# Performance work log

Hardware: AMD Instinct MI355X
Metric: run time of the kernel (lower is better)

Reference implementation:

```python
import jax, jax.numpy as jnp
import numpy as np

DIM = 1024
HEADS = 16
HEAD_DIM = DIM // HEADS
HIDDEN = 4 * DIM
SCALE = HEAD_DIM ** -0.5
MASK_VAL = -65504.0
EPS = 1e-5


def layernorm(x, scale, bias):
    mu = jnp.mean(x, axis=-1, keepdims=True)
    var = jnp.mean(jnp.square(x - mu), axis=-1, keepdims=True)
    return (x - mu) * jax.lax.rsqrt(var + EPS) * scale + bias


def setup_inputs() -> dict:
    key = jax.random.key(0)
    ks = jax.random.split(key, 10)
    B, N = 2, 2048
    s = 0.02
    return {
        "x": jax.random.normal(ks[0], (B, N, DIM), jnp.float32),
        "attention_mask": jax.random.randint(ks[1], (B, N), 0, 2) > 0,
        "attention_bias": jax.random.normal(ks[2], (N, N), jnp.float32),
        "qkv_w": jax.random.normal(ks[3], (3 * DIM, DIM), jnp.float32) * s,
        "q_bias": jnp.zeros((DIM,), jnp.float32),
        "v_bias": jnp.zeros((DIM,), jnp.float32),
        "proj_w": jax.random.normal(ks[4], (DIM, DIM), jnp.float32) * s,
        "proj_b": jnp.zeros((DIM,), jnp.float32),
        "ln1_s": jnp.ones((DIM,), jnp.float32),
        "ln1_b": jnp.zeros((DIM,), jnp.float32),
        "ln2_s": jnp.ones((DIM,), jnp.float32),
        "ln2_b": jnp.zeros((DIM,), jnp.float32),
        "fc1_w": jax.random.normal(ks[5], (HIDDEN, DIM), jnp.float32) * s,
        "fc1_b": jnp.zeros((HIDDEN,), jnp.float32),
        "fc2_w": jax.random.normal(ks[6], (DIM, HIDDEN), jnp.float32) * s,
        "fc2_b": jnp.zeros((DIM,), jnp.float32),
    }


def reference(x, attention_mask, attention_bias, qkv_w, q_bias, v_bias,
              proj_w, proj_b, ln1_s, ln1_b, ln2_s, ln2_b,
              fc1_w, fc1_b, fc2_w, fc2_b):
    B, N, C = x.shape
    h = layernorm(x, ln1_s, ln1_b)
    qkv_bias = jnp.concatenate([q_bias, jnp.zeros_like(v_bias), v_bias])
    qkv = h @ qkv_w.T + qkv_bias  # [B,N,3C]
    qkv = qkv.reshape(B, N, 3, HEADS, HEAD_DIM).transpose(2, 0, 3, 1, 4)
    q, k, v = qkv[0], qkv[1], qkv[2]  # [B,H,N,D]
    attn = jnp.einsum('bhnd,bhmd->bhnm', q * SCALE, k)
    mask = attention_mask[:, None, None, :]  # [B,1,1,N]
    attn = jnp.where(mask, MASK_VAL, attn)
    attn = attn + attention_bias[None, None]  # [1,1,N,N] bias
    attn = jax.nn.softmax(attn, axis=-1)
    out = jnp.einsum('bhnm,bhmd->bnhd', attn, v).reshape(B, N, C)
    x_attn = out @ proj_w.T + proj_b
    x = x + x_attn
    h2 = layernorm(x, ln2_s, ln2_b)
    h2 = jax.nn.gelu(h2 @ fc1_w.T + fc1_b, approximate=False)
    x = x + (h2 @ fc2_w.T + fc2_b)
    return (x, attn)
```

## Files before the change

kernel.cpp:

```cpp
#include <hip/hip_runtime.h>
#include <hip/hip_bf16.h>
#include <math.h>

#define NTOK 2048
#define DIM  1024
#define SCALE 0.125f
#define MASK_VAL -65504.0f

typedef __attribute__((ext_vector_type(8))) short bf16x8;
typedef __attribute__((ext_vector_type(4))) float floatx4;

#define MFMA16(a,b,c) __builtin_amdgcn_mfma_f32_16x16x32_bf16((a),(b),(c),0,0,0)
#define GLL16(g,l) __builtin_amdgcn_global_load_lds( \
    (const __attribute__((address_space(1))) void*)(g), \
    (__attribute__((address_space(3))) void*)(l), 16, 0, 0)

__device__ __forceinline__ short f2bf(float f) {
  union { __hip_bfloat16 h; short s; } u;
  u.h = __float2bfloat16(f);
  return u.s;
}
__device__ __forceinline__ float bf2f(short s) {
  union { short s; __hip_bfloat16 h; } u;
  u.s = s;
  return __bfloat162float(u.h);
}

__global__ __launch_bounds__(256) void cvt_bf16(const float* __restrict__ in,
                                                short* __restrict__ out) {
  size_t i = ((size_t)blockIdx.x * 256 + threadIdx.x) * 4;
  float4 v = *(const float4*)(in + i);
  short4 o;
  o.x = f2bf(v.x); o.y = f2bf(v.y); o.z = f2bf(v.z); o.w = f2bf(v.w);
  *(short4*)(out + i) = o;
}

__global__ __launch_bounds__(256) void ln_k(const float* __restrict__ x,
                                            const float* __restrict__ sc,
                                            const float* __restrict__ bi,
                                            short* __restrict__ out) {
  int row = blockIdx.x, t = threadIdx.x;
  float4 v = ((const float4*)(x + (size_t)row * DIM))[t];
  float s  = v.x + v.y + v.z + v.w;
  float s2 = v.x*v.x + v.y*v.y + v.z*v.z + v.w*v.w;
#pragma unroll
  for (int off = 32; off; off >>= 1) {
    s  += __shfl_xor(s, off);
    s2 += __shfl_xor(s2, off);
  }
  __shared__ float ps[4], ps2[4];
  if ((t & 63) == 0) { ps[t >> 6] = s; ps2[t >> 6] = s2; }
  __syncthreads();
  s  = ps[0] + ps[1] + ps[2] + ps[3];
  s2 = ps2[0] + ps2[1] + ps2[2] + ps2[3];
  float mu  = s * (1.0f / DIM);
  float inv = rsqrtf(s2 * (1.0f / DIM) - mu * mu + 1e-5f);
  float4 g = ((const float4*)sc)[t], b = ((const float4*)bi)[t];
  short4 o;
  o.x = f2bf((v.x - mu) * inv * g.x + b.x);
  o.y = f2bf((v.y - mu) * inv * g.y + b.y);
  o.z = f2bf((v.z - mu) * inv * g.z + b.z);
  o.w = f2bf((v.w - mu) * inv * g.w + b.w);
  ((short4*)(out + (size_t)row * DIM))[t] = o;
}

enum { E_QKV = 0, E_RESID = 1, E_FC1 = 2 };

template <int EPI, int K, int BN>
__global__ __launch_bounds__(256) void gemm_bt(
    const short* __restrict__ A, const short* __restrict__ B,
    const float* __restrict__ bias0, const float* __restrict__ bias1,
    const float* __restrict__ resid, float* __restrict__ outf,
    short* __restrict__ o0, short* __restrict__ o1, short* __restrict__ o2) {
  __shared__ short As[128 * 32];
  __shared__ short Bs[BN * 32];
  constexpr int MI = (BN == 128) ? 4 : 2;
  const int t = threadIdx.x;
  const int bm = blockIdx.x, bn = blockIdx.y;
  const int l = t & 63, w = t >> 6;
  const int lr = l & 15, lh = l >> 4;
  const int rowbase = (BN == 128) ? (w >> 1) * 64 : w * 32;
  const int colbase = (BN == 128) ? (w & 1) * 64 : 0;

  const short* ga = A + (size_t)(bm * 128 + (t >> 2)) * K + (t & 3) * 8;
  const short* gb = B + (size_t)(bn * BN + (t >> 2)) * K + (t & 3) * 8;
  short* la = As + t * 8;
  short* lb = Bs + t * 8;

  floatx4 acc[MI][4] = {};
  for (int kb = 0; kb < K / 32; ++kb) {
    GLL16(ga, la);
    GLL16(ga + (size_t)64 * K, la + 2048);
    GLL16(gb, lb);
    if constexpr (BN == 128) GLL16(gb + (size_t)64 * K, lb + 2048);
    ga += 32; gb += 32;
    __syncthreads();
    bf16x8 af[MI], bfr[4];
#pragma unroll
    for (int m = 0; m < MI; m++)
      af[m] = *(const bf16x8*)(As + (rowbase + m * 16 + lr) * 32 + lh * 8);
#pragma unroll
    for (int n = 0; n < 4; n++)
      bfr[n] = *(const bf16x8*)(Bs + (colbase + n * 16 + lr) * 32 + lh * 8);
#pragma unroll
    for (int m = 0; m < MI; m++)
#pragma unroll
      for (int n = 0; n < 4; n++)
        acc[m][n] = MFMA16(af[m], bfr[n], acc[m][n]);
    __syncthreads();
  }

#pragma unroll
  for (int m = 0; m < MI; m++) {
#pragma unroll
    for (int n = 0; n < 4; n++) {
#pragma unroll
      for (int j = 0; j < 4; j++) {
        int gr = bm * 128 + rowbase + m * 16 + lh * 4 + j;
        int gc = bn * BN + colbase + n * 16 + lr;
        float val = acc[m][n][j];
        if constexpr (EPI == E_QKV) {
          int which = gc >> 10, d = gc & 1023;
          int bb = gr >> 11, n_ = gr & 2047;
          size_t idx = (((size_t)bb * 16 + (d >> 6)) * NTOK + n_) * 64 + (d & 63);
          if (which == 0)      o0[idx] = f2bf((val + bias0[d]) * SCALE);
          else if (which == 1) o1[idx] = f2bf(val);
          else                 o2[idx] = f2bf(val + bias1[d]);
        } else if constexpr (EPI == E_RESID) {
          size_t idx = (size_t)gr * 1024 + gc;
          outf[idx] = val + bias0[gc] + resid[idx];
        } else {
          float u = val + bias0[gc];
          float gelu = 0.5f * u * (1.0f + erff(u * 0.70710678f));
          o0[(size_t)gr * 4096 + gc] = f2bf(gelu);
        }
      }
    }
  }
}

__global__ __launch_bounds__(256) void transpose_v(const short* __restrict__ v,
                                                   short* __restrict__ vt) {
  __shared__ short tile[64][72];
  int bh = blockIdx.x, nb = blockIdx.y, t = threadIdx.x;
  int r = t >> 2, c0 = (t & 3) * 16;
  const short* src = v + ((size_t)bh * NTOK + nb * 64 + r) * 64 + c0;
  *(bf16x8*)&tile[r][c0]     = *(const bf16x8*)src;
  *(bf16x8*)&tile[r][c0 + 8] = *(const bf16x8*)(src + 8);
  __syncthreads();
  int d = t >> 2, n0 = (t & 3) * 16;
  bf16x8 a, b;
#pragma unroll
  for (int i = 0; i < 8; i++) { a[i] = tile[n0 + i][d]; b[i] = tile[n0 + 8 + i][d]; }
  short* dst = vt + ((size_t)bh * 64 + d) * NTOK + nb * 64 + n0;
  *(bf16x8*)dst       = a;
  *(bf16x8*)(dst + 8) = b;
}

__global__ __launch_bounds__(512) void attn_k(
    const short* __restrict__ q, const short* __restrict__ k,
    const short* __restrict__ vt, const int* __restrict__ mask,
    const float* __restrict__ bias, float* __restrict__ attn_out,
    short* __restrict__ out) {
  __shared__ short S[16 * NTOK];
  __shared__ float invr[16];
  int id = blockIdx.x;
  int blk = (id & 7) * 512 + (id >> 3);
  int qt = blk & 127, bh = blk >> 7;
  int b = bh >> 4, h = bh & 15;
  int q0 = qt * 16;
  int t = threadIdx.x, l = t & 63, w = t >> 6;
  int lr = l & 15, lh = l >> 4;

  const short* qp = q + ((size_t)bh * NTOK + q0 + lr) * 64 + lh * 8;
  bf16x8 qf0 = *(const bf16x8*)qp;
  bf16x8 qf1 = *(const bf16x8*)(qp + 32);

  const int* maskb = mask + b * NTOK;
  for (int i = 0; i < 16; ++i) {
    int k0 = (w * 16 + i) * 16;
    const short* kp = k + ((size_t)bh * NTOK + k0 + lr) * 64 + lh * 8;
    bf16x8 kf0 = *(const bf16x8*)kp;
    bf16x8 kf1 = *(const bf16x8*)(kp + 32);
    floatx4 s4 = {};
    s4 = MFMA16(kf0, qf0, s4);
    s4 = MFMA16(kf1, qf1, s4);
    int m0 = k0 + lh * 4;
    int4 mk = *(const int4*)(maskb + m0);
    float4 bv = *(const float4*)(bias + (size_t)(q0 + lr) * NTOK + m0);
    short4 o;
    o.x = f2bf((mk.x ? MASK_VAL : s4[0]) + bv.x);
    o.y = f2bf((mk.y ? MASK_VAL : s4[1]) + bv.y);
    o.z = f2bf((mk.z ? MASK_VAL : s4[2]) + bv.z);
    o.w = f2bf((mk.w ? MASK_VAL : s4[3]) + bv.w);
    *(short4*)((char*)S + lr * 4096 + ((m0 * 2) ^ (lr << 4))) = o;
  }
  __syncthreads();

  int r2 = t >> 5, g = t & 31;
  char* Srow = (char*)S + r2 * 4096;
  int swz = r2 << 4;
  float mx = -3.0e38f;
#pragma unroll
  for (int i = 0; i < 8; i++) {
    int cb = (g + (i << 5)) << 4;
    bf16x8 p = *(const bf16x8*)(Srow + (cb ^ swz));
#pragma unroll
    for (int j = 0; j < 8; j++) mx = fmaxf(mx, bf2f(p[j]));
  }
#pragma unroll
  for (int off = 16; off; off >>= 1) mx = fmaxf(mx, __shfl_xor(mx, off));
  float sum = 0.f;
#pragma unroll
  for (int i = 0; i < 8; i++) {
    int cb = (g + (i << 5)) << 4;
    bf16x8* pp = (bf16x8*)(Srow + (cb ^ swz));
    bf16x8 p = *pp, e8;
#pragma unroll
    for (int j = 0; j < 8; j++) {
      float e = __expf(bf2f(p[j]) - mx);
      sum += e;
      e8[j] = f2bf(e);
    }
    *pp = e8;
  }
#pragma unroll
  for (int off = 16; off; off >>= 1) sum += __shfl_xor(sum, off);
  float inv = 1.0f / sum;
  if (g == 0) invr[r2] = inv;
  __syncthreads();

  if (w < 4) {
    floatx4 o4 = {};
    const short* vp = vt + ((size_t)bh * 64 + w * 16 + lr) * NTOK + lh * 8;
    char* Sb = (char*)S + lr * 4096;
    int pswz = lr << 4;
    for (int kt = 0; kt < 64; ++kt) {
      bf16x8 a  = *(const bf16x8*)(Sb + ((kt * 64 + lh * 16) ^ pswz));
      bf16x8 bv = *(const bf16x8*)(vp + kt * 32);
      o4 = MFMA16(a, bv, o4);
    }
#pragma unroll
    for (int j = 0; j < 4; ++j) {
      int r = lh * 4 + j;
      out[((size_t)b * NTOK + q0 + r) * DIM + h * 64 + w * 16 + lr] =
          f2bf(o4[j] * invr[r]);
    }
  } else {
    int t2 = t - 256;
    int rr = t2 >> 4, gg = t2 & 15;
    char* Sr = (char*)S + rr * 4096;
    int wswz = rr << 4;
    float vinv = invr[rr];
    float* arow = attn_out + ((size_t)bh * NTOK + q0 + rr) * NTOK;
#pragma unroll
    for (int i = 0; i < 16; ++i) {
      int c0 = (gg + (i << 4)) << 3;
      bf16x8 p = *(const bf16x8*)(Sr + ((c0 * 2) ^ wswz));
      float4 f0, f1;
      f0.x = bf2f(p[0]) * vinv; f0.y = bf2f(p[1]) * vinv;
      f0.z = bf2f(p[2]) * vinv; f0.w = bf2f(p[3]) * vinv;
      f1.x = bf2f(p[4]) * vinv; f1.y = bf2f(p[5]) * vinv;
      f1.z = bf2f(p[6]) * vinv; f1.w = bf2f(p[7]) * vinv;
      *(float4*)(arow + c0)     = f0;
      *(float4*)(arow + c0 + 4) = f1;
    }
  }
}

extern "C" void kernel_launch(void* const* d_in, const int* in_sizes, int n_in,
                              void* d_out, int out_size, void* d_ws, size_t ws_size,
                              hipStream_t stream) {
  const float* x      = (const float*)d_in[0];
  const int*   mask   = (const int*)d_in[1];
  const float* abias  = (const float*)d_in[2];
  const float* qkv_w  = (const float*)d_in[3];
  const float* q_bias = (const float*)d_in[4];
  const float* v_bias = (const float*)d_in[5];
  const float* proj_w = (const float*)d_in[6];
  const float* proj_b = (const float*)d_in[7];
  const float* ln1_s  = (const float*)d_in[8];
  const float* ln1_b  = (const float*)d_in[9];
  const float* ln2_s  = (const float*)d_in[10];
  const float* ln2_b  = (const float*)d_in[11];
  const float* fc1_w  = (const float*)d_in[12];
  const float* fc1_b  = (const float*)d_in[13];
  const float* fc2_w  = (const float*)d_in[14];
  const float* fc2_b  = (const float*)d_in[15];

  char* ws = (char*)d_ws;
  short* wq   = (short*)(ws + 0);
  short* wp   = (short*)(ws + 6291456);
  short* w1   = (short*)(ws + 8388608);
  short* w2   = (short*)(ws + 16777216);
  float* x1   = (float*)(ws + 25165824);
  short* hbuf = (short*)(ws + 41943040);
  short* qb   = (short*)(ws + 50331648);
  short* kb   = (short*)(ws + 58720256);
  short* vb   = (short*)(ws + 67108864);
  short* vtb  = (short*)(ws + 75497472);
  short* h3   = (short*)(ws + 50331648);

  float* out_x    = (float*)d_out;
  float* out_attn = (float*)d_out + 4194304;

  cvt_bf16<<<3072, 256, 0, stream>>>(qkv_w, wq);
  cvt_bf16<<<1024, 256, 0, stream>>>(proj_w, wp);
  cvt_bf16<<<4096, 256, 0, stream>>>(fc1_w, w1);
  cvt_bf16<<<4096, 256, 0, stream>>>(fc2_w, w2);

  ln_k<<<4096, 256, 0, stream>>>(x, ln1_s, ln1_b, hbuf);

  gemm_bt<E_QKV, 1024, 128><<<dim3(32, 24), 256, 0, stream>>>(
      hbuf, wq, q_bias, v_bias, nullptr, nullptr, qb, kb, vb);

  transpose_v<<<dim3(32, 32), 256, 0, stream>>>(vb, vtb);

  attn_k<<<4096, 512, 0, stream>>>(qb, kb, vtb, mask, abias, out_attn, hbuf);

  gemm_bt<E_RESID, 1024, 64><<<dim3(32, 16), 256, 0, stream>>>(
      hbuf, wp, proj_b, nullptr, x, x1, nullptr, nullptr, nullptr);

  ln_k<<<4096, 256, 0, stream>>>(x1, ln2_s, ln2_b, hbuf);

  gemm_bt<E_FC1, 1024, 128><<<dim3(32, 32), 256, 0, stream>>>(
      hbuf, w1, fc1_b, nullptr, nullptr, nullptr, h3, nullptr, nullptr);

  gemm_bt<E_RESID, 4096, 64><<<dim3(32, 16), 256, 0, stream>>>(
      h3, w2, fc2_b, nullptr, x1, out_x, nullptr, nullptr, nullptr);
}
```

Before: 1.210 ms.

## Shrink attention block to 256 threads and normalize probabilities in-place before PV

Reduces attn_k from 512 to 256 threads per block, so each wave computes twice as many score tiles and every wave does both the normalized attention-probability store and the PV MFMA. The softmax pass now writes normalized bf16 probabilities back to LDS while streaming the fp32 attention row, which removes the invr shared array and the per-row rescale at output. The XCD-aware block index remapping is also dropped. The intent is to cut thread count and synchronization overhead and let more blocks fit per CU. The trade-off is that the attn_out store and the PV work are serialized within each wave instead of running on separate waves, and the block-order change may hurt cache locality.

```diff
diff --git a/kernel.cpp b/kernel.cpp
--- a/kernel.cpp
+++ b/kernel.cpp
@@ -157,15 +157,13 @@
   *(bf16x8*)(dst + 8) = b;
 }
 
-__global__ __launch_bounds__(512) void attn_k(
+__global__ __launch_bounds__(256) void attn_k(
     const short* __restrict__ q, const short* __restrict__ k,
     const short* __restrict__ vt, const int* __restrict__ mask,
     const float* __restrict__ bias, float* __restrict__ attn_out,
     short* __restrict__ out) {
   __shared__ short S[16 * NTOK];
-  __shared__ float invr[16];
-  int id = blockIdx.x;
-  int blk = (id & 7) * 512 + (id >> 3);
+  int blk = blockIdx.x;
   int qt = blk & 127, bh = blk >> 7;
   int b = bh >> 4, h = bh & 15;
   int q0 = qt * 16;
@@ -177,8 +175,9 @@
   bf16x8 qf1 = *(const bf16x8*)(qp + 32);
 
   const int* maskb = mask + b * NTOK;
-  for (int i = 0; i < 16; ++i) {
-    int k0 = (w * 16 + i) * 16;
+  const float* biasrow = bias + (size_t)(q0 + lr) * NTOK;
+  for (int i = 0; i < 32; ++i) {
+    int k0 = (w * 32 + i) * 16;
     const short* kp = k + ((size_t)bh * NTOK + k0 + lr) * 64 + lh * 8;
     bf16x8 kf0 = *(const bf16x8*)kp;
     bf16x8 kf1 = *(const bf16x8*)(kp + 32);
@@ -187,7 +186,7 @@
     s4 = MFMA16(kf1, qf1, s4);
     int m0 = k0 + lh * 4;
     int4 mk = *(const int4*)(maskb + m0);
-    float4 bv = *(const float4*)(bias + (size_t)(q0 + lr) * NTOK + m0);
+    float4 bv = *(const float4*)(biasrow + m0);
     short4 o;
     o.x = f2bf((mk.x ? MASK_VAL : s4[0]) + bv.x);
     o.y = f2bf((mk.y ? MASK_VAL : s4[1]) + bv.y);
@@ -197,23 +196,23 @@
   }
   __syncthreads();
 
-  int r2 = t >> 5, g = t & 31;
+  int r2 = t >> 4, g = t & 15;
   char* Srow = (char*)S + r2 * 4096;
   int swz = r2 << 4;
   float mx = -3.0e38f;
 #pragma unroll
-  for (int i = 0; i < 8; i++) {
-    int cb = (g + (i << 5)) << 4;
+  for (int i = 0; i < 16; i++) {
+    int cb = (g + (i << 4)) << 4;
     bf16x8 p = *(const bf16x8*)(Srow + (cb ^ swz));
 #pragma unroll
     for (int j = 0; j < 8; j++) mx = fmaxf(mx, bf2f(p[j]));
   }
 #pragma unroll
-  for (int off = 16; off; off >>= 1) mx = fmaxf(mx, __shfl_xor(mx, off));
+  for (int off = 8; off; off >>= 1) mx = fmaxf(mx, __shfl_xor(mx, off));
   float sum = 0.f;
 #pragma unroll
-  for (int i = 0; i < 8; i++) {
-    int cb = (g + (i << 5)) << 4;
+  for (int i = 0; i < 16; i++) {
+    int cb = (g + (i << 4)) << 4;
     bf16x8* pp = (bf16x8*)(Srow + (cb ^ swz));
     bf16x8 p = *pp, e8;
 #pragma unroll
@@ -225,46 +224,44 @@
     *pp = e8;
   }
 #pragma unroll
-  for (int off = 16; off; off >>= 1) sum += __shfl_xor(sum, off);
+  for (int off = 8; off; off >>= 1) sum += __shfl_xor(sum, off);
   float inv = 1.0f / sum;
-  if (g == 0) invr[r2] = inv;
+
+  float* arow = attn_out + ((size_t)bh * NTOK + q0 + r2) * NTOK;
+#pragma unroll
+  for (int i = 0; i < 16; i++) {
+    int cb = (g + (i << 4)) << 4;
+    bf16x8* pp = (bf16x8*)(Srow + (cb ^ swz));
+    bf16x8 p = *pp, pn;
+    float4 f0, f1;
+    float pv0 = bf2f(p[0]) * inv, pv1 = bf2f(p[1]) * inv,
+          pv2 = bf2f(p[2]) * inv, pv3 = bf2f(p[3]) * inv;
+    float pv4 = bf2f(p[4]) * inv, pv5 = bf2f(p[5]) * inv,
+          pv6 = bf2f(p[6]) * inv, pv7 = bf2f(p[7]) * inv;
+    pn[0] = f2bf(pv0); pn[1] = f2bf(pv1); pn[2] = f2bf(pv2); pn[3] = f2bf(pv3);
+    pn[4] = f2bf(pv4); pn[5] = f2bf(pv5); pn[6] = f2bf(pv6); pn[7] = f2bf(pv7);
+    f0.x = pv0; f0.y = pv1; f0.z = pv2; f0.w = pv3;
+    f1.x = pv4; f1.y = pv5; f1.z = pv6; f1.w = pv7;
+    int m0 = cb >> 1;
+    *(float4*)(arow + m0)     = f0;
+    *(float4*)(arow + m0 + 4) = f1;
+    *pp = pn;
+  }
   __syncthreads();
 
-  if (w < 4) {
-    floatx4 o4 = {};
-    const short* vp = vt + ((size_t)bh * 64 + w * 16 + lr) * NTOK + lh * 8;
-    char* Sb = (char*)S + lr * 4096;
-    int pswz = lr << 4;
-    for (int kt = 0; kt < 64; ++kt) {
-      bf16x8 a  = *(const bf16x8*)(Sb + ((kt * 64 + lh * 16) ^ pswz));
-      bf16x8 bv = *(const bf16x8*)(vp + kt * 32);
-      o4 = MFMA16(a, bv, o4);
-    }
-#pragma unroll
-    for (int j = 0; j < 4; ++j) {
-      int r = lh * 4 + j;
-      out[((size_t)b * NTOK + q0 + r) * DIM + h * 64 + w * 16 + lr] =
-          f2bf(o4[j] * invr[r]);
-    }
-  } else {
-    int t2 = t - 256;
-    int rr = t2 >> 4, gg = t2 & 15;
-    char* Sr = (char*)S + rr * 4096;
-    int wswz = rr << 4;
-    float vinv = invr[rr];
-    float* arow = attn_out + ((size_t)bh * NTOK + q0 + rr) * NTOK;
-#pragma unroll
-    for (int i = 0; i < 16; ++i) {
-      int c0 = (gg + (i << 4)) << 3;
-      bf16x8 p = *(const bf16x8*)(Sr + ((c0 * 2) ^ wswz));
-      float4 f0, f1;
-      f0.x = bf2f(p[0]) * vinv; f0.y = bf2f(p[1]) * vinv;
-      f0.z = bf2f(p[2]) * vinv; f0.w = bf2f(p[3]) * vinv;
-      f1.x = bf2f(p[4]) * vinv; f1.y = bf2f(p[5]) * vinv;
-      f1.z = bf2f(p[6]) * vinv; f1.w = bf2f(p[7]) * vinv;
-      *(float4*)(arow + c0)     = f0;
-      *(float4*)(arow + c0 + 4) = f1;
-    }
+  floatx4 o4 = {};
+  const short* vp = vt + ((size_t)bh * 64 + w * 16 + lr) * NTOK + lh * 8;
+  char* Sb = (char*)S + lr * 4096;
+  int pswz = lr << 4;
+  for (int kt = 0; kt < 64; ++kt) {
+    bf16x8 a  = *(const bf16x8*)(Sb + ((kt * 64 + lh * 16) ^ pswz));
+    bf16x8 bv = *(const bf16x8*)(vp + kt * 32);
+    o4 = MFMA16(a, bv, o4);
+  }
+#pragma unroll
+  for (int j = 0; j < 4; ++j) {
+    int r = lh * 4 + j;
+    out[((size_t)b * NTOK + q0 + r) * DIM + h * 64 + w * 16 + lr] = f2bf(o4[j]);
   }
 }
 
@@ -316,7 +313,7 @@
 
   transpose_v<<<dim3(32, 32), 256, 0, stream>>>(vb, vtb);
 
-  attn_k<<<4096, 512, 0, stream>>>(qb, kb, vtb, mask, abias, out_attn, hbuf);
+  attn_k<<<4096, 256, 0, stream>>>(qb, kb, vtb, mask, abias, out_attn, hbuf);
 
   gemm_bt<E_RESID, 1024, 64><<<dim3(32, 16), 256, 0, stream>>>(
       hbuf, wp, proj_b, nullptr, x, x1, nullptr, nullptr, nullptr);
```

Measured after the change: 1.167 ms. 3.6% less time.
